# Kernel tuning notes

Hardware: AMD Instinct MI355X
Metric: run time of the kernel (lower is better)

## Reference

```python
import jax, jax.numpy as jnp
import numpy as np

# Dimensions: B graphs of NPG nodes each (equal sizes -> padding == reshape, exact)
B, NPG, DIN, H, E, DOUT, K_ORDER = 8, 4096, 128, 4, 262144, 128, 4
BETA = 0.5
N = B * NPG


def setup_inputs() -> dict:
    key = jax.random.key(0)
    k = jax.random.split(key, 12)
    s = 1.0 / np.sqrt(DIN)
    so = 1.0 / np.sqrt(H * DIN)
    x = jax.random.normal(k[0], (N, DIN), jnp.float32)
    Wq_w = jax.random.normal(k[1], (H * DIN, DIN), jnp.float32) * s
    Wq_b = jax.random.normal(k[2], (H * DIN,), jnp.float32) * 0.01
    Wk_w = jax.random.normal(k[3], (H * DIN, DIN), jnp.float32) * s
    Wk_b = jax.random.normal(k[4], (H * DIN,), jnp.float32) * 0.01
    Wo_w = jax.random.normal(k[5], (DOUT, H * DIN), jnp.float32) * so
    Wo_b = jax.random.normal(k[6], (DOUT,), jnp.float32) * 0.01
    # edges constrained within graphs (faithful to per-graph data)
    g = jax.random.randint(k[7], (E,), 0, B)
    row = g * NPG + jax.random.randint(k[8], (E,), 0, NPG)
    col = g * NPG + jax.random.randint(k[9], (E,), 0, NPG)
    edge_index = jnp.stack([row, col]).astype(jnp.int32)
    n_nodes = jnp.full((B,), NPG, jnp.int32)
    return {"x": x, "Wq_w": Wq_w, "Wq_b": Wq_b, "Wk_w": Wk_w, "Wk_b": Wk_b,
            "Wo_w": Wo_w, "Wo_b": Wo_b, "edge_index": edge_index, "n_nodes": n_nodes}


def _gcn(x, row, col):
    # x: [N,H,D]; symmetric-normalized message passing via segment sums
    deg = jax.ops.segment_sum(jnp.ones(row.shape[0], x.dtype), row, num_segments=N)
    safe = jnp.where(deg > 0, deg, 1.0)
    dis = jnp.where(deg > 0, safe ** -0.5, 0.0)
    w = (dis[row] * dis[col])[:, None, None]
    return jax.ops.segment_sum(x[col] * w, row, num_segments=N)


def _attn(qs, ks, v, n_f):
    # linear attention: out_i = (q_i . sum_j k_j v_j^T + sum_j v_j) / (q_i . sum_j k_j + n)
    q4 = qs.reshape(B, NPG, H, DIN)
    k4 = ks.reshape(B, NPG, H, DIN)
    v4 = v.reshape(B, NPG, H, DIN)
    kv = jnp.einsum('bnhd,bnhe->bhde', k4, v4)          # [B,H,D,D]
    ksum = k4.sum(axis=1)                                # [B,H,D]
    vsum = v4.sum(axis=1)                                # [B,H,D]
    num = jnp.einsum('bnhd,bhde->bnhe', q4, kv) + vsum[:, None]
    den = jnp.einsum('bnhd,bhd->bnh', q4, ksum) + n_f[:, None, None]
    return (num / den[..., None]).reshape(N, H, DIN)


def reference(x, Wq_w, Wq_b, Wk_w, Wk_b, Wo_w, Wo_b, edge_index, n_nodes):
    row, col = edge_index[0], edge_index[1]
    q = (x @ Wq_w.T + Wq_b).reshape(N, H, DIN)
    k = (x @ Wk_w.T + Wk_b).reshape(N, H, DIN)
    qs = q / jnp.linalg.norm(q, axis=2, keepdims=True)
    ks = k / jnp.linalg.norm(k, axis=2, keepdims=True)
    n_f = n_nodes.astype(x.dtype)
    xh = jnp.broadcast_to(x[:, None, :], (N, H, DIN))    # repeat over heads
    acc = xh
    cur = xh
    for _ in range(K_ORDER):
        cur = BETA * _gcn(cur, row, col) + (1.0 - BETA) * _attn(qs, ks, cur, n_f)
        acc = acc + cur
    xo = acc.reshape(N, H * DIN)
    return (xo @ Wo_w.T + Wo_b) / H
```

## Files before the change

kernel.cpp:

```cpp
#include <hip/hip_runtime.h>
#include <hip/hip_bf16.h>
#include <stdint.h>

typedef __hip_bfloat16 bf16;

#define BATCH  8
#define NPG    4096
#define DIN    128
#define NH     4
#define NEDGE  262144
#define DOUTF  128
#define KORDER 4
#define NTOT   (BATCH*NPG)
#define HD     (NH*DIN)

typedef __attribute__((ext_vector_type(8))) short short8;
typedef __attribute__((ext_vector_type(4))) float f32x4;

static __device__ __forceinline__ float b2f(bf16 v) { return __bfloat162float(v); }
static __device__ __forceinline__ float u2f(unsigned short u) {
    union { float f; unsigned int i; } c; c.i = ((unsigned int)u) << 16; return c.f;
}
static __device__ __forceinline__ unsigned short f2u(float f) {
    bf16 hb = __float2bfloat16(f);
    return *(unsigned short*)&hb;
}

__global__ void zero_kernel(uint4* p, int n) {
    int i = blockIdx.x * 256 + threadIdx.x;
    if (i < n) p[i] = uint4{0u, 0u, 0u, 0u};
}

__global__ void cvtbf_kernel(const float* __restrict__ in, bf16* __restrict__ out, int n) {
    int i = (blockIdx.x * 256 + threadIdx.x) * 8;
    if (i < n) {
        float4 a = *(const float4*)(in + i);
        float4 b = *(const float4*)(in + i + 4);
        unsigned short u[8] = { f2u(a.x), f2u(a.y), f2u(a.z), f2u(a.w),
                                f2u(b.x), f2u(b.y), f2u(b.z), f2u(b.w) };
        *(uint4*)(out + i) = *(uint4*)u;
    }
}

__global__ __launch_bounds__(256) void proj_mfma_kernel(const bf16* __restrict__ xbf,
                                                        const bf16* __restrict__ Wbf,
                                                        const float* __restrict__ bias,
                                                        bf16* __restrict__ outp,
                                                        bf16* __restrict__ outT) {
    __shared__ __align__(16) short t1[32][520];
    int n0 = blockIdx.x * 32;
    int tid = threadIdx.x;
    int lane = tid & 63, wc = tid >> 6;
    int l15 = lane & 15, quad = lane >> 4;

    f32x4 acc[2][8];
    #pragma unroll
    for (int i = 0; i < 2; i++)
        #pragma unroll
        for (int j = 0; j < 8; j++) acc[i][j] = f32x4{0.f, 0.f, 0.f, 0.f};

    #pragma unroll
    for (int ks = 0; ks < 4; ks++) {
        int kk = ks * 32 + quad * 8;
        short8 af[2];
        #pragma unroll
        for (int ti = 0; ti < 2; ti++)
            af[ti] = *(const short8*)(xbf + (size_t)(n0 + ti * 16 + l15) * DIN + kk);
        #pragma unroll
        for (int tj = 0; tj < 8; tj++) {
            short8 bfr = *(const short8*)(Wbf + (size_t)(wc * 128 + tj * 16 + l15) * DIN + kk);
            acc[0][tj] = __builtin_amdgcn_mfma_f32_16x16x32_bf16(af[0], bfr, acc[0][tj], 0, 0, 0);
            acc[1][tj] = __builtin_amdgcn_mfma_f32_16x16x32_bf16(af[1], bfr, acc[1][tj], 0, 0, 0);
        }
    }

    float bias_v[8];
    #pragma unroll
    for (int tj = 0; tj < 8; tj++) bias_v[tj] = bias[wc * 128 + tj * 16 + l15];

    #pragma unroll
    for (int ti = 0; ti < 2; ti++) {
        #pragma unroll
        for (int r = 0; r < 4; r++) {
            float s = 0.f;
            #pragma unroll
            for (int tj = 0; tj < 8; tj++) {
                float v = acc[ti][tj][r] + bias_v[tj];
                acc[ti][tj][r] = v;
                s += v * v;
            }
            s += __shfl_xor(s, 1); s += __shfl_xor(s, 2);
            s += __shfl_xor(s, 4); s += __shfl_xor(s, 8);
            float rs = rsqrtf(s);
            int node = ti * 16 + quad * 4 + r;
            #pragma unroll
            for (int tj = 0; tj < 8; tj++)
                t1[node][wc * 128 + tj * 16 + l15] = (short)f2u(acc[ti][tj][r] * rs);
        }
    }
    __syncthreads();

    if (outp) {
        #pragma unroll
        for (int u = 0; u < 8; u++) {
            int unit = u * 256 + tid;
            int nl = unit >> 6, fp = (unit & 63) * 8;
            *(uint4*)(outp + (size_t)(n0 + nl) * HD + fp) = *(uint4*)&t1[nl][fp];
        }
    }
    if (outT) {
        int b = n0 >> 12, nl0 = n0 & 4095;
        #pragma unroll
        for (int u = 0; u < 8; u++) {
            int unit = u * 256 + tid;
            int f = unit >> 2, np = (unit & 3) * 8;
            unsigned short arr[8];
            #pragma unroll
            for (int j = 0; j < 8; j++) arr[j] = (unsigned short)t1[np + j][f];
            *(uint4*)(outT + ((size_t)b * HD + f) * NPG + nl0 + np) = *(uint4*)arr;
        }
    }
}

__global__ void deg_kernel(const int* __restrict__ row, int* __restrict__ deg) {
    int e = blockIdx.x * 256 + threadIdx.x;
    if (e < NEDGE) atomicAdd(&deg[row[e]], 1);
}

__global__ void dis_kernel(const int* __restrict__ deg, float* __restrict__ dis) {
    int i = blockIdx.x * 256 + threadIdx.x;
    if (i < NTOT) {
        int d = deg[i];
        dis[i] = d > 0 ? rsqrtf((float)d) : 0.f;
    }
}

__global__ __launch_bounds__(1024) void scan1_kernel(const int* __restrict__ deg,
                                                     int* __restrict__ row_ptr, int* __restrict__ bsum) {
    __shared__ int buf[1024];
    int g = blockIdx.x, t = threadIdx.x;
    int v = deg[g * 1024 + t];
    buf[t] = v;
    __syncthreads();
    for (int off = 1; off < 1024; off <<= 1) {
        int add = (t >= off) ? buf[t - off] : 0;
        __syncthreads();
        buf[t] += add;
        __syncthreads();
    }
    row_ptr[g * 1024 + t] = buf[t] - v;
    if (t == 1023) bsum[g] = buf[1023];
}

__global__ void scan2_kernel(const int* __restrict__ bsum, int* __restrict__ boff, int* __restrict__ row_ptr) {
    int run = 0;
    for (int g = 0; g < 32; g++) { boff[g] = run; run += bsum[g]; }
    row_ptr[NTOT] = run;
}

__global__ __launch_bounds__(1024) void scan3_kernel(int* __restrict__ row_ptr, const int* __restrict__ boff) {
    row_ptr[blockIdx.x * 1024 + threadIdx.x] += boff[blockIdx.x];
}

__global__ void scatter_kernel(const int* __restrict__ row, const int* __restrict__ col,
                               const int* __restrict__ row_ptr, int* __restrict__ fill,
                               const float* __restrict__ dis,
                               int* __restrict__ col_idx, float* __restrict__ wcol) {
    int e = blockIdx.x * 256 + threadIdx.x;
    if (e < NEDGE) {
        int r = row[e], c = col[e];
        int pos = row_ptr[r] + atomicAdd(&fill[r], 1);
        col_idx[pos] = c;
        wcol[pos] = dis[c];
    }
}

__global__ __launch_bounds__(256) void rowsum_kernel(const bf16* __restrict__ T, float* __restrict__ out) {
    int row = blockIdx.x * 4 + (threadIdx.x >> 6);
    int lane = threadIdx.x & 63;
    const ushort4* p = (const ushort4*)(T + (size_t)row * NPG);
    float s = 0.f;
    #pragma unroll
    for (int wv = 0; wv < 16; wv++) {
        ushort4 u = p[lane + wv * 64];
        s += u2f(u.x) + u2f(u.y) + u2f(u.z) + u2f(u.w);
    }
    for (int off = 32; off > 0; off >>= 1) s += __shfl_down(s, off);
    if (lane == 0) out[row] = s;
}

__global__ __launch_bounds__(256) void den_kernel(const bf16* __restrict__ qs, const float* __restrict__ ksum,
                                                  const int* __restrict__ n_nodes, float* __restrict__ rden) {
    int n = blockIdx.x;
    int b = n >> 12;
    int w = threadIdx.x >> 6, lane = threadIdx.x & 63;
    int base = w * DIN;
    float p = b2f(qs[(size_t)n * HD + base + lane])      * ksum[b * HD + base + lane]
            + b2f(qs[(size_t)n * HD + base + 64 + lane]) * ksum[b * HD + base + 64 + lane];
    for (int off = 32; off > 0; off >>= 1) p += __shfl_down(p, off);
    if (lane == 0) rden[n * NH + w] = 1.0f / (p + (float)n_nodes[b]);
}

__global__ __launch_bounds__(512) void init_kernel(const bf16* __restrict__ xbf, bf16* __restrict__ cur,
                                                   bf16* __restrict__ curT, bf16* __restrict__ acc) {
    int node0 = blockIdx.x * 8;
    int t = threadIdx.x;
    int d = t & 127;
    int b = node0 >> 12, nl = node0 & 4095;
    unsigned short arr[8];
    #pragma unroll
    for (int r = 0; r < 8; r++) {
        bf16 hb = xbf[(size_t)(node0 + r) * DIN + d];
        cur[(size_t)(node0 + r) * HD + t] = hb;
        acc[(size_t)(node0 + r) * HD + t] = hb;
        arr[r] = *(unsigned short*)&hb;
    }
    *(uint4*)(curT + ((size_t)b * HD + t) * NPG + nl) = *(uint4*)arr;
}

#define KVSPLIT 8
__global__ __launch_bounds__(512, 1) void kv_mfma_kernel(const bf16* __restrict__ ksT,
                                                         const bf16* __restrict__ curT,
                                                         float* __restrict__ partial) {
    __shared__ __align__(16) short kshT[128][72];
    __shared__ __align__(16) short vshT[128][72];
    int id = blockIdx.x;
    int b = id & 7;
    int u = id >> 3;
    int h = u >> 3;
    int s = u & 7;
    int bh = b * 4 + h;
    int blk = bh * KVSPLIT + s;
    int tid = threadIdx.x;
    int lane = tid & 63;
    int w = tid >> 6;
    int wr = w >> 1, wc = w & 1;
    int d0w = wr * 32, e0w = wc * 64;
    int l15 = lane & 15, quad = lane >> 4;

    f32x4 acc[2][4];
    #pragma unroll
    for (int i = 0; i < 2; i++)
        #pragma unroll
        for (int j = 0; j < 4; j++) acc[i][j] = f32x4{0.f, 0.f, 0.f, 0.f};

    const uint4* kg = (const uint4*)(ksT + ((size_t)bh * 128) * NPG);
    const uint4* vg = (const uint4*)(curT + ((size_t)bh * 128) * NPG);
    int n0 = s * (NPG / KVSPLIT);

    for (int c = 0; c < 8; c++) {
        int nb = n0 + c * 64;
        #pragma unroll
        for (int uu = 0; uu < 2; uu++) {
            int unit = uu * 512 + tid;
            int row = unit >> 3;
            int part = unit & 7;
            int gidx = row * (NPG / 8) + (nb >> 3) + part;
            uint4 kd = kg[gidx];
            uint4 vd = vg[gidx];
            *(uint4*)&kshT[row][part * 8] = kd;
            *(uint4*)&vshT[row][part * 8] = vd;
        }
        __syncthreads();
        #pragma unroll
        for (int kkstep = 0; kkstep < 2; kkstep++) {
            int kk = kkstep * 32 + quad * 8;
            short8 af[2], bfr[4];
            #pragma unroll
            for (int ti = 0; ti < 2; ti++)
                af[ti] = *(const short8*)&kshT[d0w + ti * 16 + l15][kk];
            #pragma unroll
            for (int tj = 0; tj < 4; tj++)
                bfr[tj] = *(const short8*)&vshT[e0w + tj * 16 + l15][kk];
            #pragma unroll
            for (int ti = 0; ti < 2; ti++)
                #pragma unroll
                for (int tj = 0; tj < 4; tj++)
                    acc[ti][tj] = __builtin_amdgcn_mfma_f32_16x16x32_bf16(af[ti], bfr[tj], acc[ti][tj], 0, 0, 0);
        }
        __syncthreads();
    }
    float* p = partial + (size_t)blk * (128 * 128);
    #pragma unroll
    for (int ti = 0; ti < 2; ti++)
        #pragma unroll
        for (int tj = 0; tj < 4; tj++)
            #pragma unroll
            for (int r = 0; r < 4; r++) {
                int row = d0w + ti * 16 + quad * 4 + r;
                int col = e0w + tj * 16 + l15;
                p[row * 128 + col] = acc[ti][tj][r];
            }
}

__global__ __launch_bounds__(256) void kvredB_kernel(const float* __restrict__ partial, bf16* __restrict__ kvB) {
    __shared__ __align__(16) short t[16][136];
    int blk = blockIdx.x;
    int bh = blk >> 3;
    int e0 = (blk & 7) * 16;
    int tid = threadIdx.x;
    int el = tid & 15;
    int dc = tid >> 4;
    const float* p = partial + (size_t)bh * (KVSPLIT * 16384);
    #pragma unroll
    for (int j = 0; j < 8; j++) {
        int d = dc * 8 + j;
        int idx = d * 128 + e0 + el;
        float s = 0.f;
        #pragma unroll
        for (int sl = 0; sl < KVSPLIT; sl++) s += p[sl * 16384 + idx];
        t[el][d] = (short)f2u(s);
    }
    __syncthreads();
    int e = tid >> 4, dp = (tid & 15) * 8;
    *(uint4*)((unsigned short*)kvB + (size_t)bh * 16384 + (e0 + e) * 128 + dp) = *(uint4*)&t[e][dp];
}

__global__ __launch_bounds__(512, 2) void gcn_attn_kernel(const bf16* __restrict__ qs,
                                                          const bf16* __restrict__ kvB,
                                                          const bf16* __restrict__ cur,
                                                          const int* __restrict__ row_ptr,
                                                          const int* __restrict__ col_idx,
                                                          const float* __restrict__ wcol,
                                                          const float* __restrict__ dis,
                                                          const float* __restrict__ vsum,
                                                          const float* __restrict__ rden,
                                                          bf16* __restrict__ curN,
                                                          bf16* __restrict__ curTN,
                                                          bf16* __restrict__ accb) {
    __shared__ __align__(16) short t1[128][136];
    int id = blockIdx.x;
    int b = id & 7;
    int u = id >> 3;
    int h = u >> 5;
    int m = u & 31;
    int bh = b * 4 + h;
    int n0 = b * NPG + m * 128;
    int tid = threadIdx.x;
    int lane = tid & 63, w = tid >> 6;
    int wr = w >> 1, wc = w & 1;
    int e0w = wc * 64;
    int l15 = lane & 15, quad = lane >> 4;

    {
        int nl = tid >> 2;
        int sub = tid & 3;
        int n = n0 + nl;
        int start = row_ptr[n], end = row_ptr[n + 1];
        float g[32];
        #pragma unroll
        for (int i = 0; i < 32; i++) g[i] = 0.f;
        const bf16* gbase = cur + (size_t)h * DIN + sub * 32;
        for (int j = start; j < end; j++) {
            int c = col_idx[j];
            float wv = wcol[j];
            const uint4* p = (const uint4*)(gbase + (size_t)c * HD);
            #pragma unroll
            for (int q = 0; q < 4; q++) {
                uint4 v = p[q];
                unsigned short* sv = (unsigned short*)&v;
                #pragma unroll
                for (int k = 0; k < 8; k++) g[q * 8 + k] += wv * u2f(sv[k]);
            }
        }
        float dn = dis[n];
        int sw = (nl >> 3) & 7;
        #pragma unroll
        for (int q = 0; q < 4; q++) {
            unsigned short arr[8];
            #pragma unroll
            for (int k = 0; k < 8; k++) arr[k] = f2u(g[q * 8 + k] * dn);
            int fb = (sub * 4 + q) ^ sw;
            *(uint4*)&t1[nl][fb * 8] = *(uint4*)arr;
        }
    }

    f32x4 acc[2][4];
    #pragma unroll
    for (int i = 0; i < 2; i++)
        #pragma unroll
        for (int j = 0; j < 4; j++) acc[i][j] = f32x4{0.f, 0.f, 0.f, 0.f};

    const bf16* Aq = qs + (size_t)n0 * HD + h * DIN;
    const unsigned short* Bk = (const unsigned short*)kvB + (size_t)bh * 16384;
    #pragma unroll
    for (int ks = 0; ks < 4; ks++) {
        int kk = ks * 32 + quad * 8;
        short8 af[2], bfr[4];
        #pragma unroll
        for (int ti = 0; ti < 2; ti++)
            af[ti] = *(const short8*)(Aq + (size_t)(wr * 32 + ti * 16 + l15) * HD + kk);
        #pragma unroll
        for (int tj = 0; tj < 4; tj++)
            bfr[tj] = *(const short8*)(Bk + (e0w + tj * 16 + l15) * 128 + kk);
        #pragma unroll
        for (int ti = 0; ti < 2; ti++)
            #pragma unroll
            for (int tj = 0; tj < 4; tj++)
                acc[ti][tj] = __builtin_amdgcn_mfma_f32_16x16x32_bf16(af[ti], bfr[tj], acc[ti][tj], 0, 0, 0);
    }
    __syncthreads();

    #pragma unroll
    for (int tj = 0; tj < 4; tj++) {
        int el = e0w + tj * 16 + l15;
        float vs = vsum[b * HD + h * DIN + el];
        #pragma unroll
        for (int ti = 0; ti < 2; ti++) {
            int nlb = wr * 32 + ti * 16 + quad * 4;
            #pragma unroll
            for (int r = 0; r < 4; r++) {
                int nl = nlb + r;
                int sw = (nl >> 3) & 7;
                int pc = (((el >> 3) ^ sw) * 8) | (el & 7);
                float attnv = (acc[ti][tj][r] + vs) * rden[(size_t)(n0 + nl) * NH + h];
                float g = u2f((unsigned short)t1[nl][pc]);
                float val = 0.5f * g + 0.5f * attnv;
                t1[nl][pc] = (short)f2u(val);
            }
        }
    }
    __syncthreads();

    {
        bf16* dstn = curN + (size_t)n0 * HD + h * DIN;
        bf16* dsta = accb + (size_t)n0 * HD + h * DIN;
        #pragma unroll
        for (int uu = 0; uu < 4; uu++) {
            int unit = uu * 512 + tid;
            int nl = unit >> 4, fb = unit & 15;
            int sw = (nl >> 3) & 7;
            uint4 v = *(uint4*)&t1[nl][(fb ^ sw) * 8];
            *(uint4*)(dstn + (size_t)nl * HD + fb * 8) = v;
            unsigned short* sv = (unsigned short*)&v;
            unsigned short* ap = (unsigned short*)(dsta + (size_t)nl * HD + fb * 8);
            uint4 a = *(uint4*)ap;
            unsigned short* av = (unsigned short*)&a;
            unsigned short res[8];
            #pragma unroll
            for (int j = 0; j < 8; j++) res[j] = f2u(u2f(av[j]) + u2f(sv[j]));
            *(uint4*)ap = *(uint4*)res;
        }
    }
    {
        bf16* dstT = curTN + ((size_t)b * HD + h * DIN) * NPG + m * 128;
        #pragma unroll
        for (int uu = 0; uu < 4; uu++) {
            int unit = uu * 512 + tid;
            int fl = unit >> 4, np = (unit & 15) * 8;
            unsigned short arr[8];
            #pragma unroll
            for (int j = 0; j < 8; j++) {
                int row = np + j;
                int sw = (row >> 3) & 7;
                int pc = (((fl >> 3) ^ sw) * 8) | (fl & 7);
                arr[j] = (unsigned short)t1[row][pc];
            }
            *(uint4*)(dstT + (size_t)fl * NPG + np) = *(uint4*)arr;
        }
    }
}

__global__ __launch_bounds__(512) void out_mfma_kernel(const bf16* __restrict__ accb,
                                                       const bf16* __restrict__ Wobf,
                                                       const float* __restrict__ Wo_b,
                                                       float* __restrict__ out) {
    int n0 = blockIdx.x * 128;
    int tid = threadIdx.x;
    int lane = tid & 63, w = tid >> 6;
    int wr = w >> 1, wc = w & 1;
    int l15 = lane & 15, quad = lane >> 4;

    f32x4 acc[2][4];
    #pragma unroll
    for (int i = 0; i < 2; i++)
        #pragma unroll
        for (int j = 0; j < 4; j++) acc[i][j] = f32x4{0.f, 0.f, 0.f, 0.f};

    for (int ks = 0; ks < 16; ks++) {
        int kk = ks * 32 + quad * 8;
        short8 af[2], bfr[4];
        #pragma unroll
        for (int ti = 0; ti < 2; ti++)
            af[ti] = *(const short8*)(accb + (size_t)(n0 + wr * 32 + ti * 16 + l15) * HD + kk);
        #pragma unroll
        for (int tj = 0; tj < 4; tj++)
            bfr[tj] = *(const short8*)(Wobf + (size_t)(wc * 64 + tj * 16 + l15) * HD + kk);
        #pragma unroll
        for (int ti = 0; ti < 2; ti++)
            #pragma unroll
            for (int tj = 0; tj < 4; tj++)
                acc[ti][tj] = __builtin_amdgcn_mfma_f32_16x16x32_bf16(af[ti], bfr[tj], acc[ti][tj], 0, 0, 0);
    }

    #pragma unroll
    for (int tj = 0; tj < 4; tj++) {
        int col = wc * 64 + tj * 16 + l15;
        float bv = Wo_b[col];
        #pragma unroll
        for (int ti = 0; ti < 2; ti++) {
            int rowb = wr * 32 + ti * 16 + quad * 4;
            #pragma unroll
            for (int r = 0; r < 4; r++)
                out[(size_t)(n0 + rowb + r) * DOUTF + col] = (acc[ti][tj][r] + bv) * 0.25f;
        }
    }
}

extern "C" void kernel_launch(void* const* d_in, const int* in_sizes, int n_in,
                              void* d_out, int out_size, void* d_ws, size_t ws_size,
                              hipStream_t stream) {
    const float* x     = (const float*)d_in[0];
    const float* Wq_w  = (const float*)d_in[1];
    const float* Wq_b  = (const float*)d_in[2];
    const float* Wk_w  = (const float*)d_in[3];
    const float* Wk_b  = (const float*)d_in[4];
    const float* Wo_w  = (const float*)d_in[5];
    const float* Wo_b  = (const float*)d_in[6];
    const int*   edge  = (const int*)d_in[7];
    const int*   n_nod = (const int*)d_in[8];
    float* out = (float*)d_out;
    const int* erow = edge;
    const int* ecol = edge + NEDGE;

    char* w = (char*)d_ws;
    auto alloc = [&](size_t bytes) -> char* {
        char* p = w;
        w += (bytes + 255) & ~(size_t)255;
        return p;
    };
    bf16*  qs      = (bf16*) alloc((size_t)NTOT * HD * 2);
    bf16*  ksT     = (bf16*) alloc((size_t)NTOT * HD * 2);
    bf16*  curA    = (bf16*) alloc((size_t)NTOT * HD * 2);
    bf16*  curB    = (bf16*) alloc((size_t)NTOT * HD * 2);
    bf16*  curTA   = (bf16*) alloc((size_t)NTOT * HD * 2);
    bf16*  curTB   = (bf16*) alloc((size_t)NTOT * HD * 2);
    bf16*  accb    = (bf16*) alloc((size_t)NTOT * HD * 2);
    float* partial = (float*)alloc((size_t)32 * KVSPLIT * 16384 * 4);
    bf16*  kvB     = (bf16*) alloc((size_t)32 * 16384 * 2);
    bf16*  Wobf    = (bf16*) alloc(DOUTF * HD * 2);
    int*   degfill = (int*)  alloc(2 * NTOT * 4);
    float* dis     = (float*)alloc(NTOT * 4);
    int*   row_ptr = (int*)  alloc((NTOT + 1) * 4);
    int*   col_idx = (int*)  alloc(NEDGE * 4);
    float* wcol    = (float*)alloc(NEDGE * 4);
    float* ksum    = (float*)alloc(BATCH * HD * 4);
    float* vsum    = (float*)alloc(BATCH * HD * 4);
    float* rden    = (float*)alloc((size_t)NTOT * NH * 4);
    int*   bsum    = (int*)  alloc(32 * 4);
    int*   boff    = (int*)  alloc(32 * 4);
    int* deg  = degfill;
    int* fill = degfill + NTOT;
    bf16* xbf  = (bf16*)partial;
    bf16* Wqbf = (bf16*)((char*)partial + (8 << 20));
    bf16* Wkbf = Wqbf + (size_t)HD * DIN;

    zero_kernel<<<64, 256, 0, stream>>>((uint4*)degfill, 2 * NTOT / 4);

    cvtbf_kernel<<<NTOT * DIN / 8 / 256, 256, 0, stream>>>(x, xbf, NTOT * DIN);
    cvtbf_kernel<<<HD * DIN / 8 / 256, 256, 0, stream>>>(Wq_w, Wqbf, HD * DIN);
    cvtbf_kernel<<<HD * DIN / 8 / 256, 256, 0, stream>>>(Wk_w, Wkbf, HD * DIN);
    cvtbf_kernel<<<DOUTF * HD / 8 / 256, 256, 0, stream>>>(Wo_w, Wobf, DOUTF * HD);

    proj_mfma_kernel<<<NTOT / 32, 256, 0, stream>>>(xbf, Wqbf, Wq_b, qs, (bf16*)nullptr);
    proj_mfma_kernel<<<NTOT / 32, 256, 0, stream>>>(xbf, Wkbf, Wk_b, (bf16*)nullptr, ksT);

    deg_kernel<<<NEDGE / 256, 256, 0, stream>>>(erow, deg);
    dis_kernel<<<NTOT / 256, 256, 0, stream>>>(deg, dis);
    scan1_kernel<<<32, 1024, 0, stream>>>(deg, row_ptr, bsum);
    scan2_kernel<<<1, 1, 0, stream>>>(bsum, boff, row_ptr);
    scan3_kernel<<<32, 1024, 0, stream>>>(row_ptr, boff);
    scatter_kernel<<<NEDGE / 256, 256, 0, stream>>>(erow, ecol, row_ptr, fill, dis, col_idx, wcol);

    rowsum_kernel<<<BATCH * HD / 4, 256, 0, stream>>>(ksT, ksum);
    den_kernel<<<NTOT, 256, 0, stream>>>(qs, ksum, n_nod, rden);

    init_kernel<<<NTOT / 8, 512, 0, stream>>>(xbf, curA, curTA, accb);

    bf16* c = curA;  bf16* cT = curTA;
    bf16* cn = curB; bf16* cnT = curTB;
    for (int it = 0; it < KORDER; it++) {
        kv_mfma_kernel<<<32 * KVSPLIT, 512, 0, stream>>>(ksT, cT, partial);
        kvredB_kernel<<<256, 256, 0, stream>>>(partial, kvB);
        rowsum_kernel<<<BATCH * HD / 4, 256, 0, stream>>>(cT, vsum);
        gcn_attn_kernel<<<32 * 32, 512, 0, stream>>>(qs, kvB, c, row_ptr, col_idx, wcol, dis,
                                                     vsum, rden, cn, cnT, accb);
        bf16* t;
        t = c; c = cn; cn = t;
        t = cT; cT = cnT; cnT = t;
    }

    out_mfma_kernel<<<NTOT / 128, 512, 0, stream>>>(accb, Wobf, Wo_b, out);

    (void)in_sizes; (void)n_in; (void)out_size; (void)ws_size;
}
```

Measured before the change: 642.6 us.

## Sort gather rows by degree, prefetch edges, fuse next-iteration vsum into gcn_attn

```diff
diff --git a/kernel.cpp b/kernel.cpp
--- a/kernel.cpp
+++ b/kernel.cpp
@@ -133,6 +133,19 @@
         int d = deg[i];
         dis[i] = d > 0 ? rsqrtf((float)d) : 0.f;
     }
+}
+
+__global__ __launch_bounds__(128) void rank_kernel(const int* __restrict__ deg, int* __restrict__ perm) {
+    __shared__ int k[128];
+    int tile = blockIdx.x;
+    int t = threadIdx.x;
+    int key = deg[tile * 128 + t] * 128 + t;
+    k[t] = key;
+    __syncthreads();
+    int rank = 0;
+    #pragma unroll 8
+    for (int u = 0; u < 128; u++) rank += (k[u] < key) ? 1 : 0;
+    perm[tile * 128 + rank] = t;
 }
 
 __global__ __launch_bounds__(1024) void scan1_kernel(const int* __restrict__ deg,
@@ -323,11 +336,13 @@
                                                           const int* __restrict__ col_idx,
                                                           const float* __restrict__ wcol,
                                                           const float* __restrict__ dis,
+                                                          const int* __restrict__ perm,
                                                           const float* __restrict__ vsum,
                                                           const float* __restrict__ rden,
                                                           bf16* __restrict__ curN,
                                                           bf16* __restrict__ curTN,
-                                                          bf16* __restrict__ accb) {
+                                                          bf16* __restrict__ accb,
+                                                          float* __restrict__ vsumN) {
     __shared__ __align__(16) short t1[128][136];
     int id = blockIdx.x;
     int b = id & 7;
@@ -343,25 +358,29 @@
     int l15 = lane & 15, quad = lane >> 4;
 
     {
-        int nl = tid >> 2;
+        int rank = tid >> 2;
         int sub = tid & 3;
+        int nl = perm[(n0 >> 7) * 128 + rank];
         int n = n0 + nl;
         int start = row_ptr[n], end = row_ptr[n + 1];
         float g[32];
         #pragma unroll
         for (int i = 0; i < 32; i++) g[i] = 0.f;
         const bf16* gbase = cur + (size_t)h * DIN + sub * 32;
+        int c0 = 0; float w0 = 0.f;
+        if (start < end) { c0 = col_idx[start]; w0 = wcol[start]; }
         for (int j = start; j < end; j++) {
-            int c = col_idx[j];
-            float wv = wcol[j];
-            const uint4* p = (const uint4*)(gbase + (size_t)c * HD);
+            int c1 = 0; float w1 = 0.f;
+            if (j + 1 < end) { c1 = col_idx[j + 1]; w1 = wcol[j + 1]; }
+            const uint4* p = (const uint4*)(gbase + (size_t)c0 * HD);
             #pragma unroll
             for (int q = 0; q < 4; q++) {
                 uint4 v = p[q];
                 unsigned short* sv = (unsigned short*)&v;
                 #pragma unroll
-                for (int k = 0; k < 8; k++) g[q * 8 + k] += wv * u2f(sv[k]);
+                for (int k = 0; k < 8; k++) g[q * 8 + k] += w0 * u2f(sv[k]);
             }
+            c0 = c1; w0 = w1;
         }
         float dn = dis[n];
         int sw = (nl >> 3) & 7;
@@ -421,6 +440,22 @@
         }
     }
     __syncthreads();
+
+    {
+        int f = tid >> 2;
+        int r0 = (tid & 3) * 32;
+        float s = 0.f;
+        #pragma unroll
+        for (int r = 0; r < 32; r++) {
+            int row = r0 + r;
+            int sw = (row >> 3) & 7;
+            int pc = (((f >> 3) ^ sw) * 8) | (f & 7);
+            s += u2f((unsigned short)t1[row][pc]);
+        }
+        s += __shfl_xor(s, 1);
+        s += __shfl_xor(s, 2);
+        if ((tid & 3) == 0) atomicAdd(&vsumN[b * HD + h * DIN + f], s);
+    }
 
     {
         bf16* dstn = curN + (size_t)n0 * HD + h * DIN;
@@ -540,12 +575,14 @@
     bf16*  kvB     = (bf16*) alloc((size_t)32 * 16384 * 2);
     bf16*  Wobf    = (bf16*) alloc(DOUTF * HD * 2);
     int*   degfill = (int*)  alloc(2 * NTOT * 4);
+    int*   perm    = (int*)  alloc(NTOT * 4);
     float* dis     = (float*)alloc(NTOT * 4);
     int*   row_ptr = (int*)  alloc((NTOT + 1) * 4);
     int*   col_idx = (int*)  alloc(NEDGE * 4);
     float* wcol    = (float*)alloc(NEDGE * 4);
     float* ksum    = (float*)alloc(BATCH * HD * 4);
-    float* vsum    = (float*)alloc(BATCH * HD * 4);
+    float* vsumA   = (float*)alloc(BATCH * HD * 4);
+    float* vsumB   = (float*)alloc(BATCH * HD * 4);
     float* rden    = (float*)alloc((size_t)NTOT * NH * 4);
     int*   bsum    = (int*)  alloc(32 * 4);
     int*   boff    = (int*)  alloc(32 * 4);
@@ -567,6 +604,7 @@
 
     deg_kernel<<<NEDGE / 256, 256, 0, stream>>>(erow, deg);
     dis_kernel<<<NTOT / 256, 256, 0, stream>>>(deg, dis);
+    rank_kernel<<<NTOT / 128, 128, 0, stream>>>(deg, perm);
     scan1_kernel<<<32, 1024, 0, stream>>>(deg, row_ptr, bsum);
     scan2_kernel<<<1, 1, 0, stream>>>(bsum, boff, row_ptr);
     scan3_kernel<<<32, 1024, 0, stream>>>(row_ptr, boff);
@@ -576,18 +614,22 @@
     den_kernel<<<NTOT, 256, 0, stream>>>(qs, ksum, n_nod, rden);
 
     init_kernel<<<NTOT / 8, 512, 0, stream>>>(xbf, curA, curTA, accb);
+    rowsum_kernel<<<BATCH * HD / 4, 256, 0, stream>>>(curTA, vsumA);
 
     bf16* c = curA;  bf16* cT = curTA;
     bf16* cn = curB; bf16* cnT = curTB;
+    float* vs = vsumA;
+    float* vsN = vsumB;
     for (int it = 0; it < KORDER; it++) {
         kv_mfma_kernel<<<32 * KVSPLIT, 512, 0, stream>>>(ksT, cT, partial);
         kvredB_kernel<<<256, 256, 0, stream>>>(partial, kvB);
-        rowsum_kernel<<<BATCH * HD / 4, 256, 0, stream>>>(cT, vsum);
+        zero_kernel<<<4, 256, 0, stream>>>((uint4*)vsN, BATCH * HD / 4);
         gcn_attn_kernel<<<32 * 32, 512, 0, stream>>>(qs, kvB, c, row_ptr, col_idx, wcol, dis,
-                                                     vsum, rden, cn, cnT, accb);
+                                                     perm, vs, rden, cn, cnT, accb, vsN);
         bf16* t;
         t = c; c = cn; cn = t;
         t = cT; cT = cnT; cnT = t;
+        float* tf = vs; vs = vsN; vsN = tf;
     }
 
     out_mfma_kernel<<<NTOT / 128, 512, 0, stream>>>(accb, Wobf, Wo_b, out);
```

Result: faster. 629.0 us (-2.1%).

## Fuse value column-sum into gcn_attn via atomics and prefetch gather rows

Applied to the files above, without the earlier changes.

```diff
diff --git a/kernel.cpp b/kernel.cpp
--- a/kernel.cpp
+++ b/kernel.cpp
@@ -327,7 +327,8 @@
                                                           const float* __restrict__ rden,
                                                           bf16* __restrict__ curN,
                                                           bf16* __restrict__ curTN,
-                                                          bf16* __restrict__ accb) {
+                                                          bf16* __restrict__ accb,
+                                                          float* __restrict__ vsumN) {
     __shared__ __align__(16) short t1[128][136];
     int id = blockIdx.x;
     int b = id & 7;
@@ -351,17 +352,26 @@
         #pragma unroll
         for (int i = 0; i < 32; i++) g[i] = 0.f;
         const bf16* gbase = cur + (size_t)h * DIN + sub * 32;
+        int c0 = 0; float w0 = 0.f;
+        if (start < end) { c0 = col_idx[start]; w0 = wcol[start]; }
+        uint4 vb[4];
+        {
+            const uint4* p = (const uint4*)(gbase + (size_t)c0 * HD);
+            vb[0] = p[0]; vb[1] = p[1]; vb[2] = p[2]; vb[3] = p[3];
+        }
         for (int j = start; j < end; j++) {
-            int c = col_idx[j];
-            float wv = wcol[j];
-            const uint4* p = (const uint4*)(gbase + (size_t)c * HD);
+            int c1 = c0; float w1 = 0.f;
+            if (j + 1 < end) { c1 = col_idx[j + 1]; w1 = wcol[j + 1]; }
+            const uint4* p = (const uint4*)(gbase + (size_t)c1 * HD);
+            uint4 vn0 = p[0], vn1 = p[1], vn2 = p[2], vn3 = p[3];
             #pragma unroll
             for (int q = 0; q < 4; q++) {
-                uint4 v = p[q];
-                unsigned short* sv = (unsigned short*)&v;
+                unsigned short* sv = (unsigned short*)&vb[q];
                 #pragma unroll
-                for (int k = 0; k < 8; k++) g[q * 8 + k] += wv * u2f(sv[k]);
+                for (int k = 0; k < 8; k++) g[q * 8 + k] += w0 * u2f(sv[k]);
             }
+            vb[0] = vn0; vb[1] = vn1; vb[2] = vn2; vb[3] = vn3;
+            w0 = w1;
         }
         float dn = dis[n];
         int sw = (nl >> 3) & 7;
@@ -405,6 +415,7 @@
     for (int tj = 0; tj < 4; tj++) {
         int el = e0w + tj * 16 + l15;
         float vs = vsum[b * HD + h * DIN + el];
+        float cs = 0.f;
         #pragma unroll
         for (int ti = 0; ti < 2; ti++) {
             int nlb = wr * 32 + ti * 16 + quad * 4;
@@ -417,8 +428,12 @@
                 float g = u2f((unsigned short)t1[nl][pc]);
                 float val = 0.5f * g + 0.5f * attnv;
                 t1[nl][pc] = (short)f2u(val);
+                cs += val;
             }
         }
+        cs += __shfl_xor(cs, 16);
+        cs += __shfl_xor(cs, 32);
+        if (quad == 0) atomicAdd(&vsumN[b * HD + h * DIN + el], cs);
     }
     __syncthreads();
 
@@ -545,7 +560,8 @@
     int*   col_idx = (int*)  alloc(NEDGE * 4);
     float* wcol    = (float*)alloc(NEDGE * 4);
     float* ksum    = (float*)alloc(BATCH * HD * 4);
-    float* vsum    = (float*)alloc(BATCH * HD * 4);
+    float* vsumA   = (float*)alloc(BATCH * HD * 4);
+    float* vsumB   = (float*)alloc(BATCH * HD * 4);
     float* rden    = (float*)alloc((size_t)NTOT * NH * 4);
     int*   bsum    = (int*)  alloc(32 * 4);
     int*   boff    = (int*)  alloc(32 * 4);
@@ -576,18 +592,22 @@
     den_kernel<<<NTOT, 256, 0, stream>>>(qs, ksum, n_nod, rden);
 
     init_kernel<<<NTOT / 8, 512, 0, stream>>>(xbf, curA, curTA, accb);
+    rowsum_kernel<<<BATCH * HD / 4, 256, 0, stream>>>(curTA, vsumA);
 
     bf16* c = curA;  bf16* cT = curTA;
     bf16* cn = curB; bf16* cnT = curTB;
+    float* vs = vsumA;
+    float* vsN = vsumB;
     for (int it = 0; it < KORDER; it++) {
         kv_mfma_kernel<<<32 * KVSPLIT, 512, 0, stream>>>(ksT, cT, partial);
         kvredB_kernel<<<256, 256, 0, stream>>>(partial, kvB);
-        rowsum_kernel<<<BATCH * HD / 4, 256, 0, stream>>>(cT, vsum);
+        zero_kernel<<<4, 256, 0, stream>>>((uint4*)vsN, BATCH * HD / 4);
         gcn_attn_kernel<<<32 * 32, 512, 0, stream>>>(qs, kvB, c, row_ptr, col_idx, wcol, dis,
-                                                     vsum, rden, cn, cnT, accb);
+                                                     vs, rden, cn, cnT, accb, vsN);
         bf16* t;
         t = c; c = cn; cn = t;
         t = cT; cT = cnT; cnT = t;
+        float* tf = vs; vs = vsN; vsN = tf;
     }
 
     out_mfma_kernel<<<NTOT / 128, 512, 0, stream>>>(accb, Wobf, Wo_b, out);
```

Result: faster. 621.7 us (-3.2%).
